# Kernel optimization log

Hardware: AMD Instinct MI355X
Metric: run time of the kernel (lower is better)

Reference implementation:

```python
import jax, jax.numpy as jnp
import numpy as np

INPUT_SIZE = 1024
HIDDEN_SIZE = 1024


def setup_inputs() -> dict:
    key = jax.random.key(0)
    k1, k2, k3, k4, k5 = jax.random.split(key, 5)
    B, S, D, H = 64, 512, INPUT_SIZE, HIDDEN_SIZE
    bound_x = 1.0 / np.sqrt(D)
    bound_h = 1.0 / np.sqrt(H)
    # nn.Linear weights: (out, in) layout, uniform(-1/sqrt(in), 1/sqrt(in))
    Wx = jax.random.uniform(k1, (4 * H, D), jnp.float32, -bound_x, bound_x)
    bx = jax.random.uniform(k2, (4 * H,), jnp.float32, -bound_x, bound_x)
    Wh = jax.random.uniform(k3, (4 * H, H), jnp.float32, -bound_h, bound_h)
    bh = jax.random.uniform(k4, (4 * H,), jnp.float32, -bound_h, bound_h)
    x = jax.random.normal(k5, (B, S, D), jnp.float32)
    return {"x": x, "Wx": Wx, "bx": bx, "Wh": Wh, "bh": bh}


def _lstm_forward(x, Wx, bx, Wh, bh):
    B, S, D = x.shape
    H = Wh.shape[1]
    # Precompute the input projection for all timesteps in one big GEMM.
    x_gates = jnp.einsum('bsd,gd->bsg', x, Wx) + bx + bh  # (B, S, 4H)

    def step(carry, xg_t):
        h, c = carry
        gates = xg_t + h @ Wh.T  # (B, 4H)
        i, f, o, g = jnp.split(gates, 4, axis=1)
        i = jax.nn.sigmoid(i)
        f = jax.nn.sigmoid(f)
        o = jax.nn.sigmoid(o)
        g = jnp.tanh(g)
        c_new = f * c + i * g
        h_new = o * jnp.tanh(c_new)
        return (h_new, c_new), h_new

    h0 = jnp.zeros((B, H), x.dtype)
    c0 = jnp.zeros((B, H), x.dtype)
    (h_last, c_last), hs = jax.lax.scan(step, (h0, c0), jnp.swapaxes(x_gates, 0, 1))
    outputs = jnp.swapaxes(hs, 0, 1)  # (B, S, H)
    return outputs, (h_last, c_last)


def reference(x, Wx, bx, Wh, bh):
    return _lstm_forward(x, Wx, bx, Wh, bh)
```

## Files before the change

### kernel.cpp

```cpp
#include <hip/hip_runtime.h>


typedef short short8 __attribute__((ext_vector_type(8)));
typedef float float4v __attribute__((ext_vector_type(4)));
typedef unsigned long long u64;

__device__ __forceinline__ short f2bf(float f) {
  union { float f; unsigned u; } v; v.f = f;
  unsigned r = (v.u + 0x7fffu + ((v.u >> 16) & 1u)) >> 16;
  return (short)r;
}

__device__ __forceinline__ float sigm(float z) {
  float e = __expf(-fabsf(z));
  float p = 1.0f / (1.0f + e);
  return z >= 0.0f ? p : 1.0f - p;
}

__device__ __forceinline__ float tanh_s(float z) {
  float e = __expf(-2.0f * fabsf(z));
  float r = (1.0f - e) / (1.0f + e);
  return z >= 0.0f ? r : -r;
}

__device__ __forceinline__ void gridbar(unsigned* cnt, unsigned target, int bid, int tid) {
  __syncthreads();
  if (tid == 0) {
    unsigned g = (unsigned)(bid & 7);
    unsigned a = __hip_atomic_fetch_add(&cnt[16 + g * 16], 1u,
                    __ATOMIC_RELAXED, __HIP_MEMORY_SCOPE_AGENT);
    if ((a & 31u) == 31u) {
      unsigned r = __hip_atomic_fetch_add(&cnt[8], 1u,
                    __ATOMIC_RELAXED, __HIP_MEMORY_SCOPE_AGENT);
      if ((r & 7u) == 7u) {
        __hip_atomic_store(&cnt[0], target, __ATOMIC_RELAXED, __HIP_MEMORY_SCOPE_AGENT);
      }
    }
    while (__hip_atomic_load(&cnt[0], __ATOMIC_RELAXED, __HIP_MEMORY_SCOPE_AGENT) < target) {
      __builtin_amdgcn_s_sleep(4);
    }
  }
  __syncthreads();
}

__global__ __launch_bounds__(256) void xconv(const float* __restrict__ x,
                                             short* __restrict__ xbf) {
  const int gid = blockIdx.x * 256 + threadIdx.x;
  const long i8 = (long)gid * 8;
  const int d  = (int)(i8 & 1023);
  const int bs = (int)(i8 >> 10);
  const int s  = bs & 511;
  const int b  = bs >> 9;
  const float4v* src = (const float4v*)(x + i8);
  float4v v0 = src[0], v1 = src[1];
  short8 o;
  o[0]=f2bf(v0[0]); o[1]=f2bf(v0[1]); o[2]=f2bf(v0[2]); o[3]=f2bf(v0[3]);
  o[4]=f2bf(v1[0]); o[5]=f2bf(v1[1]); o[6]=f2bf(v1[2]); o[7]=f2bf(v1[3]);
  *(short8*)(xbf + (((size_t)(s * 64 + b)) << 10) + d) = o;
}

template <bool XBF>
__global__ __launch_bounds__(512, 2) void lstm_persist(
    const float* __restrict__ x, const short* __restrict__ xbf,
    const float* __restrict__ Wx, const float* __restrict__ bx,
    const float* __restrict__ Wh, const float* __restrict__ bh,
    float* __restrict__ out, unsigned* cnt, short* hbuf)
{
  __shared__ float red[4][64][16];
  __shared__ short hstage[64][4];

  const int tid  = threadIdx.x;
  const int bid  = blockIdx.x;
  const int lane = tid & 63;
  const int w    = tid >> 6;
  const int kq   = w & 3;
  const int mh   = w >> 2;
  const int l15  = lane & 15;
  const int lh   = lane >> 4;

  short8 bw[16];
  {
    const int n   = l15;
    const int gi  = n & 3;
    const int jj  = n >> 2;
    const int row = gi * 1024 + bid * 4 + jj;
    const float* Wsrc = (kq < 2) ? (Wx + (size_t)row * 1024 + kq * 512)
                                 : (Wh + (size_t)row * 1024 + (kq - 2) * 512);
    #pragma unroll
    for (int ks = 0; ks < 16; ++ks) {
      const float* p = Wsrc + ks * 32 + lh * 8;
      float4v v0 = *(const float4v*)p;
      float4v v1 = *(const float4v*)(p + 4);
      short8 o;
      o[0]=f2bf(v0[0]); o[1]=f2bf(v0[1]); o[2]=f2bf(v0[2]); o[3]=f2bf(v0[3]);
      o[4]=f2bf(v1[0]); o[5]=f2bf(v1[1]); o[6]=f2bf(v1[2]); o[7]=f2bf(v1[3]);
      bw[ks] = o;
    }
  }

  const int eb  = tid >> 2;
  const int ejj = tid & 3;
  const int ej  = bid * 4 + ejj;
  float bias[4] = {0.f, 0.f, 0.f, 0.f};
  if (tid < 256) {
    #pragma unroll
    for (int gi = 0; gi < 4; ++gi) bias[gi] = bx[gi * 1024 + ej] + bh[gi * 1024 + ej];
  }
  float c_reg = 0.0f, h_keep = 0.0f;

  short* hb0 = hbuf;
  short* hb1 = hbuf + 65536;

  for (int t = 0; t < 512; ++t) {
    float4v acc[2];
    acc[0] = (float4v){0.f, 0.f, 0.f, 0.f};
    acc[1] = (float4v){0.f, 0.f, 0.f, 0.f};

    if (kq < 2) {
      if (XBF) {
        const short* Ab = xbf + ((size_t)t << 16) + kq * 512 + lh * 8;
        #pragma unroll
        for (int ks = 0; ks < 16; ++ks) {
          #pragma unroll
          for (int mt = 0; mt < 2; ++mt) {
            const int b = mh * 32 + mt * 16 + l15;
            short8 a = *(const short8*)(Ab + ((size_t)b << 10) + ks * 32);
            acc[mt] = __builtin_amdgcn_mfma_f32_16x16x32_bf16(a, bw[ks], acc[mt], 0, 0, 0);
          }
        }
      } else {
        const float* Ab = x + (size_t)t * 1024 + kq * 512 + lh * 8;
        #pragma unroll
        for (int ks = 0; ks < 16; ++ks) {
          #pragma unroll
          for (int mt = 0; mt < 2; ++mt) {
            const int b = mh * 32 + mt * 16 + l15;
            const float* p = Ab + (size_t)b * 524288 + ks * 32;
            float4v v0 = *(const float4v*)p;
            float4v v1 = *(const float4v*)(p + 4);
            short8 a;
            a[0]=f2bf(v0[0]); a[1]=f2bf(v0[1]); a[2]=f2bf(v0[2]); a[3]=f2bf(v0[3]);
            a[4]=f2bf(v1[0]); a[5]=f2bf(v1[1]); a[6]=f2bf(v1[2]); a[7]=f2bf(v1[3]);
            acc[mt] = __builtin_amdgcn_mfma_f32_16x16x32_bf16(a, bw[ks], acc[mt], 0, 0, 0);
          }
        }
      }
    } else {
      const short* hb = (t & 1) ? hb1 : hb0;
      const int base = (kq - 2) * 512 + lh * 8;
      #pragma unroll
      for (int ks = 0; ks < 16; ++ks) {
        #pragma unroll
        for (int mt = 0; mt < 2; ++mt) {
          const int b = mh * 32 + mt * 16 + l15;
          const u64* p = (const u64*)(hb + ((size_t)b << 10) + base + ks * 32);
          union { u64 q[2]; short8 s; } u;
          u.q[0] = __hip_atomic_load(p,     __ATOMIC_RELAXED, __HIP_MEMORY_SCOPE_AGENT);
          u.q[1] = __hip_atomic_load(p + 1, __ATOMIC_RELAXED, __HIP_MEMORY_SCOPE_AGENT);
          acc[mt] = __builtin_amdgcn_mfma_f32_16x16x32_bf16(u.s, bw[ks], acc[mt], 0, 0, 0);
        }
      }
    }

    #pragma unroll
    for (int mt = 0; mt < 2; ++mt)
      #pragma unroll
      for (int r = 0; r < 4; ++r)
        red[kq][mh * 32 + mt * 16 + lh * 4 + r][l15] = acc[mt][r];
    __syncthreads();

    if (tid < 256) {
      float4v r0 = *(const float4v*)&red[0][eb][ejj * 4];
      float4v r1 = *(const float4v*)&red[1][eb][ejj * 4];
      float4v r2 = *(const float4v*)&red[2][eb][ejj * 4];
      float4v r3 = *(const float4v*)&red[3][eb][ejj * 4];
      const float s0 = r0[0] + r1[0] + r2[0] + r3[0] + bias[0];
      const float s1 = r0[1] + r1[1] + r2[1] + r3[1] + bias[1];
      const float s2 = r0[2] + r1[2] + r2[2] + r3[2] + bias[2];
      const float s3 = r0[3] + r1[3] + r2[3] + r3[3] + bias[3];
      const float ig = sigm(s0);
      const float fg = sigm(s1);
      const float og = sigm(s2);
      const float gg = tanh_s(s3);
      c_reg = fg * c_reg + ig * gg;
      const float hh = og * tanh_s(c_reg);
      h_keep = hh;
      out[((size_t)eb * 512 + t) * 1024 + ej] = hh;
      hstage[eb][ejj] = f2bf(hh);
    }
    __syncthreads();

    if (tid < 128) {
      unsigned v = ((const unsigned*)hstage)[tid];
      const int eb2 = tid >> 1;
      const int j0  = bid * 4 + (tid & 1) * 2;
      short* hbn = ((t + 1) & 1) ? hb1 : hb0;
      __hip_atomic_store((unsigned*)(hbn + eb2 * 1024 + j0), v,
                         __ATOMIC_RELAXED, __HIP_MEMORY_SCOPE_AGENT);
    }

    gridbar(cnt, (unsigned)t + 1u, bid, tid);
  }

  if (tid < 256) {
    const size_t BSH = (size_t)64 * 512 * 1024;
    out[BSH + (size_t)eb * 1024 + ej] = h_keep;
    out[BSH + 65536 + (size_t)eb * 1024 + ej] = c_reg;
  }
}

extern "C" void kernel_launch(void* const* d_in, const int* in_sizes, int n_in,
                              void* d_out, int out_size, void* d_ws, size_t ws_size,
                              hipStream_t stream) {
  (void)in_sizes; (void)n_in; (void)out_size;
  const float* x  = (const float*)d_in[0];
  const float* Wx = (const float*)d_in[1];
  const float* bx = (const float*)d_in[2];
  const float* Wh = (const float*)d_in[3];
  const float* bh = (const float*)d_in[4];
  float* out = (float*)d_out;

  unsigned* cnt = (unsigned*)d_ws;
  short* hbuf   = (short*)((char*)d_ws + 1024);
  short* xbf    = (short*)((char*)d_ws + 1024 + 262144);
  const size_t need_xbf = 1024u + 262144u + (size_t)64 * 512 * 1024 * 2;

  hipMemsetAsync(d_ws, 0, 1024 + 262144, stream);

  if (ws_size >= need_xbf) {
    hipLaunchKernelGGL(xconv, dim3(16384), dim3(256), 0, stream, x, xbf);
    hipLaunchKernelGGL(lstm_persist<true>, dim3(256), dim3(512), 0, stream,
                       x, xbf, Wx, bx, Wh, bh, out, cnt, hbuf);
  } else {
    hipLaunchKernelGGL(lstm_persist<false>, dim3(256), dim3(512), 0, stream,
                       x, hbuf, Wx, bx, Wh, bh, out, cnt, hbuf);
  }
}
```

Baseline: 7.755 ms.

## Split batch into two independent groups with per-group counters and LDS-staged h

Reorganizes the persistent LSTM kernel into 128 blocks of 1024 threads. Each block handles 16 hidden units for one half of the batch, and the two batch halves run as independent groups with separate h buffers and counters. The hierarchical grid barrier is replaced by a per-group monotonic counter that one wave polls while the x-projection waves proceed without waiting. The h state is copied once into swizzled LDS so the recurrent MFMA reads come from shared memory rather than repeated agent-scope global loads. This aims to cut barrier latency and global h traffic per step, but it relies on all 128 large blocks being co-resident and on ordering that uses only relaxed atomics.

```diff
diff --git a/kernel.cpp b/kernel.cpp
--- a/kernel.cpp
+++ b/kernel.cpp
@@ -21,26 +21,6 @@
   float e = __expf(-2.0f * fabsf(z));
   float r = (1.0f - e) / (1.0f + e);
   return z >= 0.0f ? r : -r;
-}
-
-__device__ __forceinline__ void gridbar(unsigned* cnt, unsigned target, int bid, int tid) {
-  __syncthreads();
-  if (tid == 0) {
-    unsigned g = (unsigned)(bid & 7);
-    unsigned a = __hip_atomic_fetch_add(&cnt[16 + g * 16], 1u,
-                    __ATOMIC_RELAXED, __HIP_MEMORY_SCOPE_AGENT);
-    if ((a & 31u) == 31u) {
-      unsigned r = __hip_atomic_fetch_add(&cnt[8], 1u,
-                    __ATOMIC_RELAXED, __HIP_MEMORY_SCOPE_AGENT);
-      if ((r & 7u) == 7u) {
-        __hip_atomic_store(&cnt[0], target, __ATOMIC_RELAXED, __HIP_MEMORY_SCOPE_AGENT);
-      }
-    }
-    while (__hip_atomic_load(&cnt[0], __ATOMIC_RELAXED, __HIP_MEMORY_SCOPE_AGENT) < target) {
-      __builtin_amdgcn_s_sleep(4);
-    }
-  }
-  __syncthreads();
 }
 
 __global__ __launch_bounds__(256) void xconv(const float* __restrict__ x,
@@ -60,30 +40,35 @@
 }
 
 template <bool XBF>
-__global__ __launch_bounds__(512, 2) void lstm_persist(
+__global__ __launch_bounds__(1024, 4) void lstm_persist(
     const float* __restrict__ x, const short* __restrict__ xbf,
     const float* __restrict__ Wx, const float* __restrict__ bx,
     const float* __restrict__ Wh, const float* __restrict__ bh,
     float* __restrict__ out, unsigned* cnt, short* hbuf)
 {
-  __shared__ float red[4][64][16];
-  __shared__ short hstage[64][4];
+  __shared__ short hS[32 * 1024];
+  __shared__ float red[4][32][68];
+  __shared__ unsigned flag;
 
   const int tid  = threadIdx.x;
   const int bid  = blockIdx.x;
+  const int g    = bid & 1;
+  const int js   = bid >> 1;
   const int lane = tid & 63;
   const int w    = tid >> 6;
-  const int kq   = w & 3;
-  const int mh   = w >> 2;
+  const int kq   = w >> 2;
+  const int rg   = w & 3;
   const int l15  = lane & 15;
   const int lh   = lane >> 4;
 
+  unsigned* cnt_g = cnt + g * 64;
+  short* hb_g = hbuf + (size_t)g * 65536;
+
   short8 bw[16];
   {
-    const int n   = l15;
-    const int gi  = n & 3;
-    const int jj  = n >> 2;
-    const int row = gi * 1024 + bid * 4 + jj;
+    const int gi  = l15 & 3;
+    const int jj  = l15 >> 2;
+    const int row = gi * 1024 + js * 16 + rg * 4 + jj;
     const float* Wsrc = (kq < 2) ? (Wx + (size_t)row * 1024 + kq * 512)
                                  : (Wh + (size_t)row * 1024 + (kq - 2) * 512);
     #pragma unroll
@@ -98,18 +83,21 @@
     }
   }
 
-  const int eb  = tid >> 2;
-  const int ejj = tid & 3;
-  const int ej  = bid * 4 + ejj;
+  const int eb  = tid >> 4;
+  const int ejj = tid & 15;
+  const int jg  = js * 16 + ejj;
   float bias[4] = {0.f, 0.f, 0.f, 0.f};
-  if (tid < 256) {
+  if (tid < 512) {
     #pragma unroll
-    for (int gi = 0; gi < 4; ++gi) bias[gi] = bx[gi * 1024 + ej] + bh[gi * 1024 + ej];
+    for (int gi = 0; gi < 4; ++gi) bias[gi] = bx[gi * 1024 + jg] + bh[gi * 1024 + jg];
   }
   float c_reg = 0.0f, h_keep = 0.0f;
 
-  short* hb0 = hbuf;
-  short* hb1 = hbuf + 65536;
+  if (tid == 0)
+    __hip_atomic_store(&flag, 0u, __ATOMIC_RELAXED, __HIP_MEMORY_SCOPE_WORKGROUP);
+  __syncthreads();
+
+  char* const hSB = (char*)hS;
 
   for (int t = 0; t < 512; ++t) {
     float4v acc[2];
@@ -118,13 +106,13 @@
 
     if (kq < 2) {
       if (XBF) {
-        const short* Ab = xbf + ((size_t)t << 16) + kq * 512 + lh * 8;
+        const short* xb = xbf + ((size_t)t << 16) + kq * 512 + lh * 8;
         #pragma unroll
         for (int ks = 0; ks < 16; ++ks) {
           #pragma unroll
           for (int mt = 0; mt < 2; ++mt) {
-            const int b = mh * 32 + mt * 16 + l15;
-            short8 a = *(const short8*)(Ab + ((size_t)b << 10) + ks * 32);
+            const int b = g * 32 + mt * 16 + l15;
+            short8 a = *(const short8*)(xb + ((size_t)b << 10) + ks * 32);
             acc[mt] = __builtin_amdgcn_mfma_f32_16x16x32_bf16(a, bw[ks], acc[mt], 0, 0, 0);
           }
         }
@@ -134,7 +122,7 @@
         for (int ks = 0; ks < 16; ++ks) {
           #pragma unroll
           for (int mt = 0; mt < 2; ++mt) {
-            const int b = mh * 32 + mt * 16 + l15;
+            const int b = g * 32 + mt * 16 + l15;
             const float* p = Ab + (size_t)b * 524288 + ks * 32;
             float4v v0 = *(const float4v*)p;
             float4v v1 = *(const float4v*)(p + 4);
@@ -145,35 +133,65 @@
           }
         }
       }
+      #pragma unroll
+      for (int mt = 0; mt < 2; ++mt)
+        #pragma unroll
+        for (int r = 0; r < 4; ++r)
+          red[kq][mt * 16 + lh * 4 + r][rg * 16 + l15] = acc[mt][r];
     } else {
-      const short* hb = (t & 1) ? hb1 : hb0;
-      const int base = (kq - 2) * 512 + lh * 8;
+      if (w == 8) {
+        const unsigned target = (unsigned)t * 64u;
+        while (__hip_atomic_load(cnt_g, __ATOMIC_RELAXED, __HIP_MEMORY_SCOPE_AGENT) < target)
+          __builtin_amdgcn_s_sleep(2);
+        if (lane == 0)
+          __hip_atomic_store(&flag, (unsigned)(t + 1), __ATOMIC_RELAXED, __HIP_MEMORY_SCOPE_WORKGROUP);
+      } else {
+        while (__hip_atomic_load(&flag, __ATOMIC_RELAXED, __HIP_MEMORY_SCOPE_WORKGROUP) < (unsigned)(t + 1))
+          __builtin_amdgcn_s_sleep(1);
+      }
+      const int tau = tid - 512;
+      const int row = tau >> 4;
+      const int sec = tau & 15;
+      const short* src = hb_g + (size_t)(t & 1) * 32768 + row * 1024 + sec * 8;
+      #pragma unroll
+      for (int i = 0; i < 8; ++i) {
+        const u64* p = (const u64*)(src + i * 128);
+        union { u64 q[2]; short8 s; } u;
+        u.q[0] = __hip_atomic_load(p,     __ATOMIC_RELAXED, __HIP_MEMORY_SCOPE_AGENT);
+        u.q[1] = __hip_atomic_load(p + 1, __ATOMIC_RELAXED, __HIP_MEMORY_SCOPE_AGENT);
+        const unsigned byte = (((unsigned)row << 11) + sec * 16 + i * 256)
+                              ^ ((unsigned)(row & 7) << 4);
+        *(short8*)(hSB + byte) = u.s;
+      }
+    }
+    __syncthreads();
+
+    if (kq >= 2) {
+      const unsigned cb = (unsigned)((kq - 2) * 1024 + lh * 16);
+      const unsigned xr = (unsigned)((l15 & 7) << 4);
       #pragma unroll
       for (int ks = 0; ks < 16; ++ks) {
         #pragma unroll
         for (int mt = 0; mt < 2; ++mt) {
-          const int b = mh * 32 + mt * 16 + l15;
-          const u64* p = (const u64*)(hb + ((size_t)b << 10) + base + ks * 32);
-          union { u64 q[2]; short8 s; } u;
-          u.q[0] = __hip_atomic_load(p,     __ATOMIC_RELAXED, __HIP_MEMORY_SCOPE_AGENT);
-          u.q[1] = __hip_atomic_load(p + 1, __ATOMIC_RELAXED, __HIP_MEMORY_SCOPE_AGENT);
-          acc[mt] = __builtin_amdgcn_mfma_f32_16x16x32_bf16(u.s, bw[ks], acc[mt], 0, 0, 0);
+          const unsigned byte = (((unsigned)(mt * 16 + l15) << 11) + cb + ks * 64) ^ xr;
+          short8 a = *(const short8*)(hSB + byte);
+          acc[mt] = __builtin_amdgcn_mfma_f32_16x16x32_bf16(a, bw[ks], acc[mt], 0, 0, 0);
         }
       }
-    }
-
-    #pragma unroll
-    for (int mt = 0; mt < 2; ++mt)
-      #pragma unroll
-      for (int r = 0; r < 4; ++r)
-        red[kq][mh * 32 + mt * 16 + lh * 4 + r][l15] = acc[mt][r];
+      #pragma unroll
+      for (int mt = 0; mt < 2; ++mt)
+        #pragma unroll
+        for (int r = 0; r < 4; ++r)
+          red[kq][mt * 16 + lh * 4 + r][rg * 16 + l15] = acc[mt][r];
+    }
     __syncthreads();
 
-    if (tid < 256) {
-      float4v r0 = *(const float4v*)&red[0][eb][ejj * 4];
-      float4v r1 = *(const float4v*)&red[1][eb][ejj * 4];
-      float4v r2 = *(const float4v*)&red[2][eb][ejj * 4];
-      float4v r3 = *(const float4v*)&red[3][eb][ejj * 4];
+    if (tid < 512) {
+      const int base = (ejj >> 2) * 16 + (ejj & 3) * 4;
+      const float4v r0 = *(const float4v*)&red[0][eb][base];
+      const float4v r1 = *(const float4v*)&red[1][eb][base];
+      const float4v r2 = *(const float4v*)&red[2][eb][base];
+      const float4v r3 = *(const float4v*)&red[3][eb][base];
       const float s0 = r0[0] + r1[0] + r2[0] + r3[0] + bias[0];
       const float s1 = r0[1] + r1[1] + r2[1] + r3[1] + bias[1];
       const float s2 = r0[2] + r1[2] + r2[2] + r3[2] + bias[2];
@@ -185,27 +203,24 @@
       c_reg = fg * c_reg + ig * gg;
       const float hh = og * tanh_s(c_reg);
       h_keep = hh;
-      out[((size_t)eb * 512 + t) * 1024 + ej] = hh;
-      hstage[eb][ejj] = f2bf(hh);
+      out[((size_t)(g * 32 + eb) * 512 + t) * 1024 + jg] = hh;
+      unsigned hv = (unsigned)(unsigned short)f2bf(hh);
+      unsigned nb = (unsigned)__shfl_xor((int)hv, 1, 64);
+      if ((ejj & 1) == 0) {
+        unsigned vv = hv | (nb << 16);
+        unsigned* dst = (unsigned*)(hb_g + (size_t)((t + 1) & 1) * 32768 + eb * 1024 + jg);
+        __hip_atomic_store(dst, vv, __ATOMIC_RELAXED, __HIP_MEMORY_SCOPE_AGENT);
+      }
     }
     __syncthreads();
-
-    if (tid < 128) {
-      unsigned v = ((const unsigned*)hstage)[tid];
-      const int eb2 = tid >> 1;
-      const int j0  = bid * 4 + (tid & 1) * 2;
-      short* hbn = ((t + 1) & 1) ? hb1 : hb0;
-      __hip_atomic_store((unsigned*)(hbn + eb2 * 1024 + j0), v,
-                         __ATOMIC_RELAXED, __HIP_MEMORY_SCOPE_AGENT);
-    }
-
-    gridbar(cnt, (unsigned)t + 1u, bid, tid);
-  }
-
-  if (tid < 256) {
+    if (tid == 0)
+      __hip_atomic_fetch_add(cnt_g, 1u, __ATOMIC_RELAXED, __HIP_MEMORY_SCOPE_AGENT);
+  }
+
+  if (tid < 512) {
     const size_t BSH = (size_t)64 * 512 * 1024;
-    out[BSH + (size_t)eb * 1024 + ej] = h_keep;
-    out[BSH + 65536 + (size_t)eb * 1024 + ej] = c_reg;
+    out[BSH + (size_t)(g * 32 + eb) * 1024 + jg] = h_keep;
+    out[BSH + 65536 + (size_t)(g * 32 + eb) * 1024 + jg] = c_reg;
   }
 }
 
@@ -229,10 +244,10 @@
 
   if (ws_size >= need_xbf) {
     hipLaunchKernelGGL(xconv, dim3(16384), dim3(256), 0, stream, x, xbf);
-    hipLaunchKernelGGL(lstm_persist<true>, dim3(256), dim3(512), 0, stream,
+    hipLaunchKernelGGL(lstm_persist<true>, dim3(128), dim3(1024), 0, stream,
                        x, xbf, Wx, bx, Wh, bh, out, cnt, hbuf);
   } else {
-    hipLaunchKernelGGL(lstm_persist<false>, dim3(256), dim3(512), 0, stream,
+    hipLaunchKernelGGL(lstm_persist<false>, dim3(128), dim3(1024), 0, stream,
                        x, hbuf, Wx, bx, Wh, bh, out, cnt, hbuf);
   }
 }
```

Result: faster. 7.471 ms (-3.7%).
